# Performance work log

Measured on AMD Instinct MI355X. Metric: run time of the kernel, lower is better.

The kernel has to match this reference:

```python
import jax, jax.numpy as jnp
import numpy as np

T = 1_500_000   # traindata rows
N = 2_000_000   # neighbor rows
n = 1_048_576   # layer's n (divisible by 4)
m = 1           # layer's m (sort column)
NEG_INIT = -100000.0


def setup_inputs() -> dict:
    key = jax.random.key(0)
    k1, k2, k3, k4, k5 = jax.random.split(key, 5)
    feats = jax.random.normal(k1, (T, 3), dtype=jnp.float32)
    # col 0: node ID = arange(T); cols 1:4: features
    traindata = jnp.concatenate([jnp.arange(T, dtype=jnp.float32)[:, None], feats], axis=1)
    ids = jax.random.randint(k2, (N,), 0, T).astype(jnp.float32)      # col 0: IDs into traindata
    sortcol = jax.random.normal(k3, (N,), dtype=jnp.float32)          # col m=1: sort key
    mid = jax.random.normal(k4, (N, 2), dtype=jnp.float32)            # cols 2,3
    flag = jax.random.randint(k5, (N,), 0, 10).astype(jnp.float32)
    neighbor = jnp.stack([ids, sortcol, mid[:, 0], mid[:, 1], flag], axis=1)
    return {"traindata": traindata, "neighbor": neighbor}


def reference(traindata, neighbor):
    # tf.nn.top_k(bt, k=full, sorted=True) == stable descending sort
    bt = neighbor[:, m]
    order = jnp.argsort(-bt)          # stable -> ties keep original index order, like top_k
    data = neighbor[order]
    new_neighbor = data[neighbor.shape[0] - n:]   # bottom-n rows [n, 5]

    # rows of new_neighbor whose flag (col 4) == 0: append their IDs, gathered from the
    # ORIGINAL neighbor col 0 (as in the source), padded with 3 zero feature cols.
    zero_mask = new_neighbor[:, 4] == 0
    idx = jnp.nonzero(zero_mask, size=n, fill_value=0)[0]        # static-size for jit
    valid = jnp.arange(n) < jnp.sum(zero_mask)
    rev_ids = jnp.where(valid, neighbor[idx, 0], jnp.float32(-1.0))  # -1 never matches a real ID
    rev = jnp.concatenate([rev_ids[:, None], jnp.zeros((n, 3), neighbor.dtype)], axis=1)
    td = jnp.concatenate([traindata, rev], axis=0)               # [T+n, 4]
    tdlist = td[:, 0]

    # tp[e] = FIRST index where tdlist == new_neighbor[e, 0]
    # stable argsort + searchsorted(left) gives the smallest original index among equals
    sort_idx = jnp.argsort(tdlist)
    sv = tdlist[sort_idx]
    pos = jnp.searchsorted(sv, new_neighbor[:, 0], side='left')
    tp = sort_idx[pos]                                           # [n]

    max_ = jnp.max(td[tp, 1:], axis=1)                           # [n] row-wise feature max
    flags = new_neighbor[:, 4]

    G = n // 4
    tp_g = tp.reshape(G, 4)
    max_g = max_.reshape(G, 4)
    flag_g = flags.reshape(G, 4)

    # sequential 4-step recurrence per group (mirrors the j-loop with tf.cond):
    # update iff (flag != 0) == (max_ > maxmin)
    maxmin = jnp.full((G,), NEG_INIT, dtype=max_.dtype)
    maxindex = jnp.full((G,), -100, dtype=tp.dtype)
    for j in range(4):
        re1 = flag_g[:, j] != 0
        gt = max_g[:, j] > maxmin
        re = re1 == gt
        maxmin = jnp.where(re, max_g[:, j], maxmin)
        maxindex = jnp.where(re, tp_g[:, j], maxindex)

    # gather surviving traindata rows (clip guards the never-updated -100 sentinel,
    # which would be an error in the original TF graph)
    out = td[jnp.clip(maxindex, 0, td.shape[0] - 1)]             # [G, 4]
    return out
```

## Files before the change

kernel.cpp:

```cpp
#include <hip/hip_runtime.h>
#include <stdint.h>

#define T_ROWS 1500000
#define N_ROWS 2000000
#define N_SEL  1048576
#define G_CNT  (N_SEL/4)
#define LB     (N_ROWS - N_SEL)
#define TILE   4096
#define NBLK   ((N_ROWS + TILE - 1)/TILE)
#define THREADS 512
#define WAVES  8
#define WTILE  (TILE/WAVES)
#define WROUNDS (WTILE/64)
#define BINS   256
#define CHUNK  ((NBLK + WAVES - 1)/WAVES)
#define NB_MX  ((T_ROWS + THREADS - 1)/THREADS)

static_assert((uint64_t)NBLK * TILE >= N_ROWS, "tile coverage");
static_assert(T_ROWS < (1 << 21), "tp fits 21 bits");
static_assert((LB * 4) % 16 == 0, "finalize uint4 alignment");

__global__ __launch_bounds__(THREADS) void build_all(
        const float* __restrict__ nb, const float* __restrict__ td,
        uint64_t* __restrict__ codes, float* __restrict__ mxtab,
        uint32_t* __restrict__ gT) {
    const int b = blockIdx.x;
    if (b >= NBLK) {
        int i = (b - NBLK) * THREADS + threadIdx.x;
        if (i < T_ROWS) {
            float4 r = *(const float4*)(td + (size_t)i * 4);
            mxtab[i] = fmaxf(r.y, fmaxf(r.z, r.w));
        }
        return;
    }
    __shared__ uint32_t h[BINS];
    const int t = threadIdx.x;
    if (t < BINS) h[t] = 0;
    __syncthreads();
    const int base = b * TILE;
    #pragma unroll
    for (int r = 0; r < TILE / THREADS; ++r) {
        int i = base + r * THREADS + t;
        if (i < N_ROWS) {
            const float* row = nb + (size_t)i * 5;
            uint32_t u = __float_as_uint(row[1]);
            uint32_t ku = (u & 0x80000000u) ? ~u : (u | 0x80000000u);
            uint32_t kd = ~ku;
            uint32_t tp = (uint32_t)(int)row[0];
            uint32_t fl = (row[4] != 0.0f) ? 1u : 0u;
            codes[i] = ((uint64_t)kd << 32) | (fl << 21) | tp;
            atomicAdd(&h[kd & (BINS - 1)], 1u);
        }
    }
    __syncthreads();
    if (t < BINS) gT[(size_t)b * BINS + t] = h[t];
}

template <int SHIFT32>
__global__ __launch_bounds__(THREADS) void radix_hist_u(
        const uint64_t* __restrict__ src, uint32_t* __restrict__ gT) {
    __shared__ uint32_t h[BINS];
    const int t = threadIdx.x;
    if (t < BINS) h[t] = 0;
    __syncthreads();
    const int base = blockIdx.x * TILE;
    const uint32_t* s32 = (const uint32_t*)src;
    #pragma unroll
    for (int r = 0; r < TILE / THREADS; ++r) {
        int i = base + r * THREADS + t;
        if (i < N_ROWS)
            atomicAdd(&h[(s32[2 * (size_t)i + 1] >> SHIFT32) & (BINS - 1)], 1u);
    }
    __syncthreads();
    if (t < BINS) gT[(size_t)blockIdx.x * BINS + t] = h[t];
}

template <int SHIFT32>
__global__ __launch_bounds__(THREADS) void radix_hist_s(
        const uint64_t* __restrict__ src, uint32_t* __restrict__ gT) {
    __shared__ uint32_t h[BINS];
    const int t = threadIdx.x;
    const int lane = t & 63;
    if (t < BINS) h[t] = 0;
    __syncthreads();
    const int base = blockIdx.x * TILE;
    const uint32_t* s32 = (const uint32_t*)src;
    #pragma unroll
    for (int r = 0; r < TILE / THREADS; ++r) {
        int i = base + r * THREADS + t;
        bool active = (i < N_ROWS);
        uint32_t d = 0;
        if (active) d = (s32[2 * (size_t)i + 1] >> SHIFT32) & (BINS - 1);
        uint64_t m = __ballot(active ? 1 : 0);
        #pragma unroll
        for (int bb = 0; bb < 8; ++bb) {
            uint64_t x = __ballot((active && ((d >> bb) & 1u)) ? 1 : 0);
            m = ((d >> bb) & 1u) ? (m & x) : (m & ~x);
        }
        int ldr = __ffsll((unsigned long long)m) - 1;
        if (active && lane == ldr) atomicAdd(&h[d], (uint32_t)__popcll(m));
    }
    __syncthreads();
    if (t < BINS) gT[(size_t)blockIdx.x * BINS + t] = h[t];
}

template <int SHIFT, bool LAST>
__global__ __launch_bounds__(THREADS) void radix_scatter(
        const uint64_t* __restrict__ src, uint64_t* __restrict__ dst,
        uint32_t* __restrict__ dst32, const uint32_t* __restrict__ gT) {
    __shared__ uint64_t tileS[TILE];
    __shared__ uint32_t cnt32[BINS * WAVES];
    __shared__ uint32_t writeBase[BINS];
    __shared__ uint32_t wpT[WAVES], wpL[WAVES];
    uint32_t* pB0 = (uint32_t*)tileS;

    const int t = threadIdx.x;
    const int lane = t & 63;
    const int w = t >> 6;
    const int blk = blockIdx.x;
    const int base = blk * TILE;
    const int tileCount = (N_ROWS - base < TILE) ? (N_ROWS - base) : TILE;

    uint32_t lcv = 0;
    if (t < BINS) lcv = gT[(size_t)blk * BINS + t];

    #pragma unroll
    for (int k = t; k < BINS * WAVES; k += THREADS) cnt32[k] = 0u;
    __syncthreads();

    uint64_t creg[WROUNDS];
    uint32_t meta[WROUNDS];
    const uint64_t below = (lane == 0) ? 0ull : (~0ull >> (64 - lane));
    #pragma unroll
    for (int r = 0; r < WROUNDS; ++r) {
        int idx = base + w * WTILE + r * 64 + lane;
        bool active = (idx < N_ROWS);
        uint64_t c = active ? src[idx] : 0ull;
        creg[r] = c;
        uint32_t d = (uint32_t)(c >> SHIFT) & (BINS - 1);
        uint64_t m = __ballot(active ? 1 : 0);
        #pragma unroll
        for (int bb = 0; bb < 8; ++bb) {
            uint64_t x = __ballot((active && ((d >> bb) & 1u)) ? 1 : 0);
            m = ((d >> bb) & 1u) ? (m & x) : (m & ~x);
        }
        int ldr = __ffsll((unsigned long long)m) - 1;
        uint32_t cnt = (uint32_t)__popcll(m);
        uint32_t rank = (uint32_t)__popcll(m & below);
        meta[r] = rank | ((uint32_t)(ldr < 0 ? 0 : ldr) << 8) | (cnt << 16);
        if (active && lane == ldr)
            atomicAdd(&cnt32[d * WAVES + w], cnt);
    }

    {
        uint32_t totw[4] = {0, 0, 0, 0}, rpw[4] = {0, 0, 0, 0};
        int i0 = w * CHUNK;
        int i1 = (i0 + CHUNK < NBLK) ? (i0 + CHUNK) : NBLK;
        for (int i = i0; i < i1; ++i) {
            uint4 v = *(const uint4*)(gT + (size_t)i * BINS + lane * 4);
            totw[0] += v.x; totw[1] += v.y; totw[2] += v.z; totw[3] += v.w;
            if (i < blk) { rpw[0] += v.x; rpw[1] += v.y; rpw[2] += v.z; rpw[3] += v.w; }
        }
        *(uint4*)(pB0 + (size_t)w * BINS + lane * 4) =
            make_uint4(totw[0], totw[1], totw[2], totw[3]);
        *(uint4*)(pB0 + 2048 + (size_t)w * BINS + lane * 4) =
            make_uint4(rpw[0], rpw[1], rpw[2], rpw[3]);
    }
    __syncthreads();

    uint32_t tot = 0, rp = 0;
    if (t < BINS) {
        #pragma unroll
        for (int wv = 0; wv < WAVES; ++wv) {
            tot += pB0[wv * BINS + t];
            rp  += pB0[2048 + wv * BINS + t];
        }
    }
    uint32_t sT = tot, sL = lcv;
    #pragma unroll
    for (int off = 1; off < 64; off <<= 1) {
        uint32_t aT = __shfl_up(sT, off, 64);
        uint32_t aL = __shfl_up(sL, off, 64);
        if (lane >= off) { sT += aT; sL += aL; }
    }
    if (lane == 63) { wpT[w] = sT; wpL[w] = sL; }
    __syncthreads();
    uint32_t exT = sT - tot, exL = sL - lcv;
    #pragma unroll
    for (int wv = 0; wv < WAVES; ++wv) if (wv < w) { exT += wpT[wv]; exL += wpL[wv]; }

    if (t < BINS) {
        writeBase[t] = exT + rp - exL;
        uint32_t run = exL;
        #pragma unroll
        for (int wv = 0; wv < WAVES; ++wv) {
            uint32_t c0 = cnt32[t * WAVES + wv];
            cnt32[t * WAVES + wv] = run;
            run += c0;
        }
    }
    __syncthreads();

    #pragma unroll
    for (int r = 0; r < WROUNDS; ++r) {
        int idx = base + w * WTILE + r * 64 + lane;
        bool active = (idx < N_ROWS);
        uint64_t c = creg[r];
        uint32_t d = (uint32_t)(c >> SHIFT) & (BINS - 1);
        uint32_t mt = meta[r];
        uint32_t rank = mt & 0xFFu;
        int ldr = (int)((mt >> 8) & 0xFFu);
        uint32_t cnt = mt >> 16;
        uint32_t before = 0;
        if (active && lane == ldr)
            before = atomicAdd(&cnt32[d * WAVES + w], cnt);
        before = __shfl(before, ldr, 64);
        if (active) tileS[before + rank] = c;
    }
    __syncthreads();

    #pragma unroll
    for (int r = 0; r < TILE / THREADS; ++r) {
        int p = r * THREADS + t;
        if (p < tileCount) {
            uint64_t c = tileS[p];
            uint32_t d = (uint32_t)(c >> SHIFT) & (BINS - 1);
            uint32_t g = writeBase[d] + p;
            if (!LAST) {
                dst[(size_t)g] = c;
            } else if (g >= LB) {
                dst32[g] = (uint32_t)c;
            }
        }
    }
}

__global__ void finalize(const uint32_t* __restrict__ pay, const float* __restrict__ td,
                         const float* __restrict__ mxtab, float* __restrict__ out) {
    int g = blockIdx.x * 256 + threadIdx.x;
    if (g >= G_CNT) return;
    uint4 p4 = *(const uint4*)(pay + LB + (size_t)g * 4);
    uint32_t cs[4] = {p4.x, p4.y, p4.z, p4.w};
    float maxmin = -100000.0f;
    int maxindex = -100;
    #pragma unroll
    for (int j = 0; j < 4; ++j) {
        int tp = (int)(cs[j] & 0x1FFFFFu);
        bool re1 = ((cs[j] >> 21) & 1u) != 0u;
        float mx = mxtab[tp];
        bool gt = (mx > maxmin);
        if (re1 == gt) { maxmin = mx; maxindex = tp; }
    }
    int mi = maxindex < 0 ? 0 : maxindex;
    float4 row = *(const float4*)(td + (size_t)mi * 4);
    *(float4*)(out + (size_t)g * 4) = row;
}

extern "C" void kernel_launch(void* const* d_in, const int* in_sizes, int n_in,
                              void* d_out, int out_size, void* d_ws, size_t ws_size,
                              hipStream_t stream) {
    const float* td = (const float*)d_in[0];
    const float* nb = (const float*)d_in[1];
    float* out = (float*)d_out;
    uint8_t* ws = (uint8_t*)d_ws;

    float*    mxtab = (float*)(ws);
    uint32_t* gT    = (uint32_t*)(ws + (size_t)6 * 1024 * 1024);
    uint64_t* A     = (uint64_t*)(ws + (size_t)8 * 1024 * 1024);
    uint64_t* B     = (uint64_t*)(ws + (size_t)24 * 1024 * 1024);

    build_all<<<NBLK + NB_MX, THREADS, 0, stream>>>(nb, td, A, mxtab, gT);

    radix_scatter<32, false><<<NBLK, THREADS, 0, stream>>>(A, B, nullptr, gT);

    radix_hist_u<8><<<NBLK, THREADS, 0, stream>>>(B, gT);
    radix_scatter<40, false><<<NBLK, THREADS, 0, stream>>>(B, A, nullptr, gT);

    radix_hist_u<16><<<NBLK, THREADS, 0, stream>>>(A, gT);
    radix_scatter<48, false><<<NBLK, THREADS, 0, stream>>>(A, B, nullptr, gT);

    radix_hist_s<24><<<NBLK, THREADS, 0, stream>>>(B, gT);
    radix_scatter<56, true><<<NBLK, THREADS, 0, stream>>>(B, nullptr, (uint32_t*)A, gT);

    finalize<<<(G_CNT + 255) / 256, 256, 0, stream>>>((const uint32_t*)A, td, mxtab, out);
}
```

Baseline: 142.1 us.

## Replace per-block redundant histogram prefix reduction with cooperative bin-major scan and spin barrier

Radix histograms are now stored bin-major. In each scatter pass, the first 256 blocks each exclusive-scan one bin row in place and bump a global done counter. All blocks spin on that counter before reading their prefix, local count and total directly. Previously every block re-reduced the whole block×bin histogram table to get its offsets. This removes that redundant global read traffic, but it relies on all 489 blocks being co-resident for the spin wait to be safe.

```diff
diff --git a/kernel.cpp b/kernel.cpp
--- a/kernel.cpp
+++ b/kernel.cpp
@@ -8,24 +8,27 @@
 #define LB     (N_ROWS - N_SEL)
 #define TILE   4096
 #define NBLK   ((N_ROWS + TILE - 1)/TILE)
+#define NBLK1  (NBLK + 1)
 #define THREADS 512
 #define WAVES  8
 #define WTILE  (TILE/WAVES)
 #define WROUNDS (WTILE/64)
 #define BINS   256
-#define CHUNK  ((NBLK + WAVES - 1)/WAVES)
 #define NB_MX  ((T_ROWS + THREADS - 1)/THREADS)
 
 static_assert((uint64_t)NBLK * TILE >= N_ROWS, "tile coverage");
 static_assert(T_ROWS < (1 << 21), "tp fits 21 bits");
 static_assert((LB * 4) % 16 == 0, "finalize uint4 alignment");
+static_assert(3 * 256 >= NBLK, "all blocks co-resident (spin safety)");
 
 __global__ __launch_bounds__(THREADS) void build_all(
         const float* __restrict__ nb, const float* __restrict__ td,
         uint64_t* __restrict__ codes, float* __restrict__ mxtab,
-        uint32_t* __restrict__ gT) {
+        uint32_t* __restrict__ gH, uint32_t* __restrict__ done) {
     const int b = blockIdx.x;
     if (b >= NBLK) {
+        if (b == NBLK && threadIdx.x == 0)
+            __hip_atomic_store(done, 0u, __ATOMIC_RELAXED, __HIP_MEMORY_SCOPE_AGENT);
         int i = (b - NBLK) * THREADS + threadIdx.x;
         if (i < T_ROWS) {
             float4 r = *(const float4*)(td + (size_t)i * 4);
@@ -53,12 +56,12 @@
         }
     }
     __syncthreads();
-    if (t < BINS) gT[(size_t)b * BINS + t] = h[t];
+    if (t < BINS) gH[(size_t)t * NBLK1 + b] = h[t];
 }
 
 template <int SHIFT32>
 __global__ __launch_bounds__(THREADS) void radix_hist_u(
-        const uint64_t* __restrict__ src, uint32_t* __restrict__ gT) {
+        const uint64_t* __restrict__ src, uint32_t* __restrict__ gH) {
     __shared__ uint32_t h[BINS];
     const int t = threadIdx.x;
     if (t < BINS) h[t] = 0;
@@ -72,12 +75,12 @@
             atomicAdd(&h[(s32[2 * (size_t)i + 1] >> SHIFT32) & (BINS - 1)], 1u);
     }
     __syncthreads();
-    if (t < BINS) gT[(size_t)blockIdx.x * BINS + t] = h[t];
+    if (t < BINS) gH[(size_t)t * NBLK1 + blockIdx.x] = h[t];
 }
 
 template <int SHIFT32>
 __global__ __launch_bounds__(THREADS) void radix_hist_s(
-        const uint64_t* __restrict__ src, uint32_t* __restrict__ gT) {
+        const uint64_t* __restrict__ src, uint32_t* __restrict__ gH) {
     __shared__ uint32_t h[BINS];
     const int t = threadIdx.x;
     const int lane = t & 63;
@@ -101,18 +104,18 @@
         if (active && lane == ldr) atomicAdd(&h[d], (uint32_t)__popcll(m));
     }
     __syncthreads();
-    if (t < BINS) gT[(size_t)blockIdx.x * BINS + t] = h[t];
+    if (t < BINS) gH[(size_t)t * NBLK1 + blockIdx.x] = h[t];
 }
 
 template <int SHIFT, bool LAST>
 __global__ __launch_bounds__(THREADS) void radix_scatter(
         const uint64_t* __restrict__ src, uint64_t* __restrict__ dst,
-        uint32_t* __restrict__ dst32, const uint32_t* __restrict__ gT) {
+        uint32_t* __restrict__ dst32, uint32_t* __restrict__ gH,
+        uint32_t* __restrict__ done, uint32_t target) {
     __shared__ uint64_t tileS[TILE];
     __shared__ uint32_t cnt32[BINS * WAVES];
     __shared__ uint32_t writeBase[BINS];
     __shared__ uint32_t wpT[WAVES], wpL[WAVES];
-    uint32_t* pB0 = (uint32_t*)tileS;
 
     const int t = threadIdx.x;
     const int lane = t & 63;
@@ -121,12 +124,34 @@
     const int base = blk * TILE;
     const int tileCount = (N_ROWS - base < TILE) ? (N_ROWS - base) : TILE;
 
-    uint32_t lcv = 0;
-    if (t < BINS) lcv = gT[(size_t)blk * BINS + t];
-
     #pragma unroll
     for (int k = t; k < BINS * WAVES; k += THREADS) cnt32[k] = 0u;
     __syncthreads();
+
+    if (blk < BINS && w == 0) {
+        uint32_t* row = gH + (size_t)blk * NBLK1;
+        uint32_t carry = 0;
+        for (int b0 = 0; b0 < NBLK; b0 += 64) {
+            int i = b0 + lane;
+            uint32_t v = (i < NBLK) ? row[i] : 0u;
+            uint32_t s = v;
+            #pragma unroll
+            for (int off = 1; off < 64; off <<= 1) {
+                uint32_t a = __shfl_up(s, off, 64);
+                if (lane >= off) s += a;
+            }
+            if (i < NBLK)
+                __hip_atomic_store(&row[i], s - v + carry,
+                                   __ATOMIC_RELAXED, __HIP_MEMORY_SCOPE_AGENT);
+            carry += __shfl(s, 63, 64);
+        }
+        if (lane == 0) {
+            __hip_atomic_store(&row[NBLK], carry,
+                               __ATOMIC_RELAXED, __HIP_MEMORY_SCOPE_AGENT);
+            __hip_atomic_fetch_add(done, 1u,
+                                   __ATOMIC_RELEASE, __HIP_MEMORY_SCOPE_AGENT);
+        }
+    }
 
     uint64_t creg[WROUNDS];
     uint32_t meta[WROUNDS];
@@ -151,32 +176,23 @@
         if (active && lane == ldr)
             atomicAdd(&cnt32[d * WAVES + w], cnt);
     }
-
-    {
-        uint32_t totw[4] = {0, 0, 0, 0}, rpw[4] = {0, 0, 0, 0};
-        int i0 = w * CHUNK;
-        int i1 = (i0 + CHUNK < NBLK) ? (i0 + CHUNK) : NBLK;
-        for (int i = i0; i < i1; ++i) {
-            uint4 v = *(const uint4*)(gT + (size_t)i * BINS + lane * 4);
-            totw[0] += v.x; totw[1] += v.y; totw[2] += v.z; totw[3] += v.w;
-            if (i < blk) { rpw[0] += v.x; rpw[1] += v.y; rpw[2] += v.z; rpw[3] += v.w; }
-        }
-        *(uint4*)(pB0 + (size_t)w * BINS + lane * 4) =
-            make_uint4(totw[0], totw[1], totw[2], totw[3]);
-        *(uint4*)(pB0 + 2048 + (size_t)w * BINS + lane * 4) =
-            make_uint4(rpw[0], rpw[1], rpw[2], rpw[3]);
-    }
-    __syncthreads();
-
-    uint32_t tot = 0, rp = 0;
+    __syncthreads();
+
+    if (t == 0) {
+        while (__hip_atomic_load(done, __ATOMIC_ACQUIRE, __HIP_MEMORY_SCOPE_AGENT) < target) {}
+    }
+    __syncthreads();
+
+    uint32_t rp = 0, lc = 0, tot = 0;
     if (t < BINS) {
-        #pragma unroll
-        for (int wv = 0; wv < WAVES; ++wv) {
-            tot += pB0[wv * BINS + t];
-            rp  += pB0[2048 + wv * BINS + t];
-        }
-    }
-    uint32_t sT = tot, sL = lcv;
+        uint32_t* row = gH + (size_t)t * NBLK1;
+        rp  = __hip_atomic_load(&row[blk], __ATOMIC_RELAXED, __HIP_MEMORY_SCOPE_AGENT);
+        uint32_t nxt = __hip_atomic_load(&row[blk + 1], __ATOMIC_RELAXED, __HIP_MEMORY_SCOPE_AGENT);
+        tot = __hip_atomic_load(&row[NBLK], __ATOMIC_RELAXED, __HIP_MEMORY_SCOPE_AGENT);
+        lc = nxt - rp;
+    }
+
+    uint32_t sT = tot, sL = lc;
     #pragma unroll
     for (int off = 1; off < 64; off <<= 1) {
         uint32_t aT = __shfl_up(sT, off, 64);
@@ -185,7 +201,7 @@
     }
     if (lane == 63) { wpT[w] = sT; wpL[w] = sL; }
     __syncthreads();
-    uint32_t exT = sT - tot, exL = sL - lcv;
+    uint32_t exT = sT - tot, exL = sL - lc;
     #pragma unroll
     for (int wv = 0; wv < WAVES; ++wv) if (wv < w) { exT += wpT[wv]; exL += wpL[wv]; }
 
@@ -265,22 +281,23 @@
     uint8_t* ws = (uint8_t*)d_ws;
 
     float*    mxtab = (float*)(ws);
-    uint32_t* gT    = (uint32_t*)(ws + (size_t)6 * 1024 * 1024);
+    uint32_t* gH    = (uint32_t*)(ws + (size_t)6 * 1024 * 1024);
+    uint32_t* done  = (uint32_t*)(ws + (size_t)6 * 1024 * 1024 + 512 * 1024);
     uint64_t* A     = (uint64_t*)(ws + (size_t)8 * 1024 * 1024);
     uint64_t* B     = (uint64_t*)(ws + (size_t)24 * 1024 * 1024);
 
-    build_all<<<NBLK + NB_MX, THREADS, 0, stream>>>(nb, td, A, mxtab, gT);
-
-    radix_scatter<32, false><<<NBLK, THREADS, 0, stream>>>(A, B, nullptr, gT);
-
-    radix_hist_u<8><<<NBLK, THREADS, 0, stream>>>(B, gT);
-    radix_scatter<40, false><<<NBLK, THREADS, 0, stream>>>(B, A, nullptr, gT);
-
-    radix_hist_u<16><<<NBLK, THREADS, 0, stream>>>(A, gT);
-    radix_scatter<48, false><<<NBLK, THREADS, 0, stream>>>(A, B, nullptr, gT);
-
-    radix_hist_s<24><<<NBLK, THREADS, 0, stream>>>(B, gT);
-    radix_scatter<56, true><<<NBLK, THREADS, 0, stream>>>(B, nullptr, (uint32_t*)A, gT);
+    build_all<<<NBLK + NB_MX, THREADS, 0, stream>>>(nb, td, A, mxtab, gH, done);
+
+    radix_scatter<32, false><<<NBLK, THREADS, 0, stream>>>(A, B, nullptr, gH, done, 256u);
+
+    radix_hist_u<8><<<NBLK, THREADS, 0, stream>>>(B, gH);
+    radix_scatter<40, false><<<NBLK, THREADS, 0, stream>>>(B, A, nullptr, gH, done, 512u);
+
+    radix_hist_u<16><<<NBLK, THREADS, 0, stream>>>(A, gH);
+    radix_scatter<48, false><<<NBLK, THREADS, 0, stream>>>(A, B, nullptr, gH, done, 768u);
+
+    radix_hist_s<24><<<NBLK, THREADS, 0, stream>>>(B, gH);
+    radix_scatter<56, true><<<NBLK, THREADS, 0, stream>>>(B, nullptr, (uint32_t*)A, gH, done, 1024u);
 
     finalize<<<(G_CNT + 255) / 256, 256, 0, stream>>>((const uint32_t*)A, td, mxtab, out);
 }
```

Result: slower. 170.7 us (+20.1%).
